# Kernel optimization log

Hardware: AMD Instinct MI355X
Metric: run time of the kernel (lower is better)

## Reference

```python
import jax, jax.numpy as jnp
import numpy as np

# static video/block geometry (matches grid_sizes = [12, 30, 50], block_layout = (3, 5, 10))
F_, H_, W_ = 12, 30, 50
FB, HB, WB = 3, 5, 10
P1, P2, P3 = F_ // FB, H_ // HB, W_ // WB      # (4, 6, 5) -> 120 tokens per block
NB = FB * HB * WB                               # 150 blocks
B = 1
N = F_ * H_ * W_                                # 18000 tokens
DIM, NH = 1536, 12
HD = DIM // NH                                  # 128
CC = HD // 2                                    # 64 rotary pairs
SPLITS = (CC - 2 * (CC // 3), CC // 3, CC // 3) # (22, 21, 21) per torch split
EPS = 1e-6
MAXP = max(F_, H_, W_)


def _block_weight():
    # BlockDistanceConv3D with transform='linear': 1 - d/dmax, column-normalized (sum over dim=0)
    f, i, j = np.meshgrid(np.arange(FB), np.arange(HB), np.arange(WB), indexing='ij')
    centers = np.stack([f.ravel() + 0.5, i.ravel() + 0.5, j.ravel() + 0.5], 1).astype(np.float64)
    d = np.linalg.norm(centers[:, None] - centers[None, :], axis=-1)
    mat = 1.0 - d / d.max()
    mat = mat / mat.sum(axis=0, keepdims=True)
    return jnp.asarray(mat, jnp.float32)        # [NB, NB]

W_BLK = _block_weight()


def setup_inputs():
    key = jax.random.key(0)
    ks = jax.random.split(key, 10)
    x = jax.random.normal(ks[0], (B, N, DIM), jnp.float32)
    seq_lens = jnp.full((B,), N, jnp.int32)
    grid_sizes = jnp.tile(jnp.array([[F_, H_, W_]], jnp.int32), (B, 1))
    # rope freqs table [MAXP, CC]: per-axis sub-tables of widths SPLITS, base 1e4
    cols = []
    for sz in SPLITS:
        inv = 1.0 / (10000.0 ** (np.arange(sz, dtype=np.float64) / sz))
        cols.append(np.arange(MAXP)[:, None] * inv[None, :])
    ang = np.concatenate(cols, axis=1)
    freqs_cos = jnp.asarray(np.cos(ang), jnp.float32)
    freqs_sin = jnp.asarray(np.sin(ang), jnp.float32)
    s = 0.02
    wq = jax.random.normal(ks[1], (DIM, DIM), jnp.float32) * s
    wk = jax.random.normal(ks[2], (DIM, DIM), jnp.float32) * s
    wv = jax.random.normal(ks[3], (DIM, DIM), jnp.float32) * s
    wo = jax.random.normal(ks[4], (DIM, DIM), jnp.float32) * s
    bq = jax.random.normal(ks[5], (DIM,), jnp.float32) * 0.01
    bk = jax.random.normal(ks[6], (DIM,), jnp.float32) * 0.01
    bv = jax.random.normal(ks[7], (DIM,), jnp.float32) * 0.01
    bo = jnp.zeros((DIM,), jnp.float32)
    nq_w = 1.0 + 0.1 * jax.random.normal(ks[8], (DIM,), jnp.float32)
    nk_w = 1.0 + 0.1 * jax.random.normal(ks[9], (DIM,), jnp.float32)
    return dict(x=x, seq_lens=seq_lens, grid_sizes=grid_sizes,
                freqs_cos=freqs_cos, freqs_sin=freqs_sin,
                wq=wq, bq=bq, wk=wk, bk=bk, wv=wv, bv=bv, wo=wo, bo=bo,
                nq_w=nq_w, nk_w=nk_w)


def _rmsnorm(t, w):
    return t * jax.lax.rsqrt(jnp.mean(t * t, -1, keepdims=True) + EPS) * w


def _pos_tab(tab):
    # expand per-axis freq table into per-token table [N, CC] (f-major, then h, then w)
    c0, c1 = SPLITS[0], SPLITS[0] + SPLITS[1]
    f = jnp.broadcast_to(tab[:F_, :c0][:, None, None, :], (F_, H_, W_, SPLITS[0]))
    h = jnp.broadcast_to(tab[:H_, c0:c1][None, :, None, :], (F_, H_, W_, SPLITS[1]))
    w = jnp.broadcast_to(tab[:W_, c1:][None, None, :, :], (F_, H_, W_, SPLITS[2]))
    return jnp.concatenate([f, h, w], -1).reshape(N, CC)


def _rope(t, cos, sin):
    # complex multiply on interleaved pairs, real arithmetic: (x0+ix1)*(c+is)
    tr = t.reshape(B, N, NH, CC, 2)
    x0, x1 = tr[..., 0], tr[..., 1]
    c = cos[None, :, None, :]
    s = sin[None, :, None, :]
    return jnp.stack([x0 * c - x1 * s, x0 * s + x1 * c], -1).reshape(B, N, NH, HD)


def _to_blocks(t):
    # 'b (fb p1 hb p2 wb p3) h d -> (b h) (fb hb wb) (p1 p2 p3) d'
    t = t.reshape(B, FB, P1, HB, P2, WB, P3, NH, HD)
    t = t.transpose(0, 7, 1, 3, 5, 2, 4, 6, 8)
    return t.reshape(B * NH, NB, P1 * P2 * P3, HD)


def reference(x, seq_lens, grid_sizes, freqs_cos, freqs_sin,
              wq, bq, wk, bk, wv, bv, wo, bo, nq_w, nk_w):
    # qkv projections (float32 throughout, as torch upcasts q/k/v to float)
    q = x @ wq.T + bq
    k = x @ wk.T + bk
    v = x @ wv.T + bv
    # RMSNorm over full dim, then relu + eps (linear-attention positivity)
    q = jax.nn.relu(_rmsnorm(q, nq_w)) + EPS
    k = jax.nn.relu(_rmsnorm(k, nk_w)) + EPS
    q = q.reshape(B, N, NH, HD)
    k = k.reshape(B, N, NH, HD)
    v = v.reshape(B, N, NH, HD)
    pc, ps = _pos_tab(freqs_cos), _pos_tab(freqs_sin)
    q_rope = _rope(q, pc, ps)
    k_rope = _rope(k, pc, ps)
    qb, kb, vb, qrb, krb = map(_to_blocks, (q, k, v, q_rope, k_rope))
    # per-block linear attention state: kv[b,n] = k_rope^T @ v
    kv = jnp.einsum('bnpd,bnpe->bnde', krb, vb)           # [B*NH, NB, HD, HD]
    kv = jnp.einsum('oi,bide->bode', W_BLK, kv)            # block-distance mixing (1x1 conv)
    # normalizer: block_mix(q @ sum_p k)
    ksum = kb.sum(axis=2)                                  # [B*NH, NB, HD]
    qk = jnp.einsum('bnpd,bnd->bnp', qb, ksum)             # [B*NH, NB, P]
    norm = jnp.einsum('oi,bip->bop', W_BLK, qk)[..., None] + EPS
    out = jnp.einsum('bnpd,bnde->bnpe', qrb, kv) / norm    # [B*NH, NB, P, HD]
    # '(b h) n p d -> b (fb p1 hb p2 wb p3) (h d)'
    out = out.reshape(B, NH, FB, HB, WB, P1, P2, P3, HD)
    out = out.transpose(0, 2, 5, 3, 6, 4, 7, 1, 8).reshape(B, N, DIM)
    return out @ wo.T + bo
```

## Files before the change

kernel.cpp:

```cpp
#include <hip/hip_runtime.h>
#include <stdint.h>


typedef unsigned short u16;
typedef unsigned int   u32;

typedef _Float16 f16x8 __attribute__((ext_vector_type(8)));
typedef float    f32x4 __attribute__((ext_vector_type(4)));

#define N_TOK 18000
#define MPAD  18176
#define DIMD  1536
#define NHH   12
#define HD    128
#define CCH   64
#define QKVN  4608
#define NBLK  150
#define PBLK  120
#define EPSF  1e-6f

#define DEVFN static __device__ __forceinline__
#define AS1 __attribute__((address_space(1)))
#define AS3 __attribute__((address_space(3)))

DEVFN u16 f2h(float f){ _Float16 h = (_Float16)f; return __builtin_bit_cast(u16, h); }
DEVFN float h2f(u16 u){ _Float16 h = __builtin_bit_cast(_Float16, u); return (float)h; }
DEVFN int2 pack4h(float a,float b,float c,float d){
  int2 r;
  r.x = (int)((u32)f2h(a) | ((u32)f2h(b)<<16));
  r.y = (int)((u32)f2h(c) | ((u32)f2h(d)<<16));
  return r;
}
DEVFN int4 packi4(float4 lo4, float4 hi4){
  int2 lo = pack4h(lo4.x, lo4.y, lo4.z, lo4.w);
  int2 hi = pack4h(hi4.x, hi4.y, hi4.z, hi4.w);
  int4 r; r.x=lo.x; r.y=lo.y; r.z=hi.x; r.w=hi.y;
  return r;
}

DEVFN void gl_lds16(const u16* g, u16* l){
  __builtin_amdgcn_global_load_lds((const AS1 void*)g, (AS3 void*)l, 16, 0, 0);
}

DEVFN f32x4 mf(f16x8 a, f16x8 b, f32x4 c){
  return __builtin_amdgcn_mfma_f32_16x16x32_f16(a, b, c, 0, 0, 0);
}

DEVFN int tok_of(int b, int p){
  int fb = b/50, hb = (b/10)%5, wb = b%10;
  int p1 = p/30; int pr = p - p1*30; int p2 = pr/5, p3 = pr - p2*5;
  return (fb*4 + p1)*1500 + (hb*6 + p2)*50 + (wb*5 + p3);
}
DEVFN void tok_pos(int b, int p, int& tok, int& f, int& h2, int& w2){
  int fb = b/50, hb = (b/10)%5, wb = b%10;
  int p1 = p/30; int pr = p - p1*30; int p2 = pr/5, p3 = pr - p2*5;
  f = fb*4 + p1; h2 = hb*6 + p2; w2 = wb*5 + p3;
  tok = (f*30 + h2)*50 + w2;
}


__global__ void conv_x_k(const float* __restrict__ x, u16* __restrict__ xh){
  const long i = ((long)blockIdx.x*256 + threadIdx.x)*8;
  if (i >= (long)MPAD*DIMD) return;
  if (i < (long)N_TOK*DIMD){
    const float4 a = *(const float4*)(x + i);
    const float4 b = *(const float4*)(x + i + 4);
    *(int4*)(xh + i) = packi4(a, b);
  } else {
    *(int4*)(xh + i) = make_int4(0,0,0,0);
  }
}

__global__ void conv_w_k(const float* __restrict__ wq, const float* __restrict__ wk,
                         const float* __restrict__ wv, const float* __restrict__ wo,
                         const float* __restrict__ bq, const float* __restrict__ bk,
                         const float* __restrict__ bv,
                         u16* __restrict__ wqkvb, u16* __restrict__ wob, float* __restrict__ bqkv){
  const long i = (long)blockIdx.x*256 + threadIdx.x;
  const long idx = i*4;
  const long SQ = (long)DIMD*DIMD;
  const long WQKV = 3*SQ;
  if (idx < WQKV){
    const float* src = (idx < SQ) ? (wq + idx) : (idx < 2*SQ ? wk + (idx - SQ) : wv + (idx - 2*SQ));
    const float4 v = *(const float4*)src;
    *(int2*)(wqkvb + idx) = pack4h(v.x, v.y, v.z, v.w);
  } else if (idx < WQKV + SQ){
    const long j = idx - WQKV;
    const float4 v = *(const float4*)(wo + j);
    *(int2*)(wob + j) = pack4h(v.x, v.y, v.z, v.w);
  }
  if (i < 3*DIMD) bqkv[i] = (i < DIMD) ? bq[i] : (i < 2*DIMD ? bk[i - DIMD] : bv[i - 2*DIMD]);
}

__global__ void wblk_k(float* __restrict__ wblk, u16* __restrict__ wh){
  __shared__ double cs[NBLK];
  const int t = threadIdx.x;
  const double dmax = sqrt(101.0);
  if (t < NBLK){
    const int fi = t/50, hi = (t/10)%5, wi = t%10;
    double s = 0.0;
    for (int o = 0; o < NBLK; o++){
      const int fo = o/50, ho = (o/10)%5, wo = o%10;
      const int df = fo-fi, dh = ho-hi, dw = wo-wi;
      s += 1.0 - sqrt((double)(df*df + dh*dh + dw*dw))/dmax;
    }
    cs[t] = s;
  }
  __syncthreads();
  for (int idx = t; idx < NBLK*NBLK; idx += 256){
    const int o = idx/NBLK, i = idx%NBLK;
    const int fo = o/50, ho = (o/10)%5, wo = o%10;
    const int fi = i/50, hi = (i/10)%5, wi = i%10;
    const int df = fo-fi, dh = ho-hi, dw = wo-wi;
    const double v = 1.0 - sqrt((double)(df*df + dh*dh + dw*dw))/dmax;
    wblk[idx] = (float)(v / cs[i]);
  }
  for (int idx = t; idx < 160*160; idx += 256){
    const int o = idx/160, i = idx%160;
    u16 hv = 0;
    if (o < NBLK && i < NBLK){
      const int fo = o/50, ho = (o/10)%5, wo = o%10;
      const int fi = i/50, hi = (i/10)%5, wi = i%10;
      const int df = fo-fi, dh = ho-hi, dw = wo-wi;
      const double v = 1.0 - sqrt((double)(df*df + dh*dh + dw*dw))/dmax;
      hv = f2h((float)(v / cs[i]));
    }
    wh[idx] = hv;
  }
}


#define STG_A(bB, kt, h) { const int ko_ = (kt)*64 + (h)*32; \
  gl_lds16(Aat + offA0 + ko_, lds + (bB)*32768 + (h)*8192 + t*8); \
  gl_lds16(Aat + offA1 + ko_, lds + (bB)*32768 + (h)*8192 + t*8 + 4096); }
#define STG_B(bB, kt, h) { const int ko_ = (kt)*64 + (h)*32; \
  gl_lds16(Bat + offB0 + ko_, lds + (bB)*32768 + 16384 + (h)*8192 + t*8); \
  gl_lds16(Bat + offB1 + ko_, lds + (bB)*32768 + 16384 + (h)*8192 + t*8 + 4096); }
#define VMC(n) asm volatile("s_waitcnt vmcnt(" #n ")" ::: "memory")
#define BARR() __builtin_amdgcn_s_barrier()
#define LGK(n) { asm volatile("s_waitcnt lgkmcnt(" #n ")" ::: "memory"); \
                 __builtin_amdgcn_sched_barrier(0); }

#define RD_A4(dst, bB, kk, mlo) { \
  _Pragma("unroll") for (int i_=0;i_<4;i_++) \
    dst[i_] = *(const f16x8*)(lds + (bB)*32768 + (kk)*8192 + arow + ((mlo)+i_)*512); }
#define RD_B4(dst, bB, kk) { \
  _Pragma("unroll") for (int i_=0;i_<4;i_++) \
    dst[i_] = *(const f16x8*)(lds + (bB)*32768 + 16384 + (kk)*8192 + brow + i_*512); }
#define MM4(mlo, aR, bR) { \
  __builtin_amdgcn_s_setprio(1); \
  _Pragma("unroll") for (int i_=0;i_<4;i_++){ \
    acc[(mlo)+i_][0] = mf(aR[i_], bR[0], acc[(mlo)+i_][0]); \
    acc[(mlo)+i_][1] = mf(aR[i_], bR[1], acc[(mlo)+i_][1]); \
    acc[(mlo)+i_][2] = mf(aR[i_], bR[2], acc[(mlo)+i_][2]); \
    acc[(mlo)+i_][3] = mf(aR[i_], bR[3], acc[(mlo)+i_][3]); } \
  __builtin_amdgcn_s_setprio(0); }

#define TILE4(bB, S1, S2, S3, S4, VM) { \
  RD_A4(aA, bB, 0, 0); RD_B4(bX, bB, 0); RD_A4(aB, bB, 0, 4); \
  S1; LGK(4); MM4(0, aA, bX); BARR(); \
  RD_A4(aA, bB, 1, 0); RD_B4(bY, bB, 1); \
  S2; LGK(8); MM4(4, aB, bX); BARR(); \
  RD_A4(aB, bB, 1, 4); \
  S3; LGK(4); MM4(0, aA, bY); BARR(); \
  S4; VM; LGK(0); MM4(4, aB, bY); BARR(); }

DEVFN void gemm256_core(const u16* __restrict__ Aat, const u16* __restrict__ Bat,
                        u16* lds, long row0, long col0, int K, f32x4 (&acc)[8][4]){
  const int t = threadIdx.x;
  const int lane = t&63, lr = lane&15;
  const int q = lane>>4;
  const int w = t>>6, wr = w>>2, wc = w&3;
  const int slot8 = (q ^ ((lr>>1)&3))*8;
  const int arow = (wr*128 + lr)*32 + slot8;
  const int brow = (wc*64 + lr)*32 + slot8;
  const int s1 = t + 512;
  const int r0 = t>>2, r1 = s1>>2;
  const int g0 = ((t&3)  ^ ((r0>>1)&3))*8;
  const int g1 = ((s1&3) ^ ((r1>>1)&3))*8;
  const long offA0 = (row0 + r0)*(long)K + g0, offA1 = (row0 + r1)*(long)K + g1;
  const long offB0 = (col0 + r0)*(long)K + g0, offB1 = (col0 + r1)*(long)K + g1;

  f16x8 aA[4], aB[4], bX[4], bY[4];
  STG_A(0,0,0); STG_B(0,0,0); STG_A(0,0,1); STG_B(0,0,1);
  STG_A(1,1,0); STG_B(1,1,0);
  VMC(4); BARR();

  const int NIT = K/128;
#pragma unroll 1
  for (int j = 0; j < NIT-1; ++j){
    const int c1 = 2*j+1, p0 = 2*j+2, p1 = 2*j+3;
    TILE4(0, STG_A(1,c1,1), STG_B(1,c1,1), STG_A(0,p0,0), STG_B(0,p0,0), VMC(4));
    TILE4(1, STG_A(0,p0,1), STG_B(0,p0,1), STG_A(1,p1,0), STG_B(1,p1,0), VMC(4));
  }
  { const int cL1 = 2*(K/128)-1;
    TILE4(0, STG_A(1,cL1,1), STG_B(1,cL1,1), (void)0, (void)0, VMC(0));
    TILE4(1, (void)0, (void)0, (void)0, (void)0, (void)0);
  }
}

__global__ __launch_bounds__(512, 2) void gemm_qkv256(const u16* __restrict__ A, const u16* __restrict__ B,
                                                      const float* __restrict__ bias,
                                                      u16* __restrict__ qb, u16* __restrict__ kb,
                                                      u16* __restrict__ vb){
  __shared__ u16 lds[65536];
  const int bn = blockIdx.x, bm = blockIdx.y;
  const long row0 = (long)bm*256, col0 = (long)bn*256;
  f32x4 acc[8][4] = {};
  gemm256_core(A, B, lds, row0, col0, DIMD, acc);

  const int t = threadIdx.x, lane = t&63, lr = lane&15, q = lane>>4;
  const int w = t>>6, wr = w>>2, wc = w&3;
  const int which = bn/6;
  u16* dst = (which == 0) ? qb : (which == 1 ? kb : vb);
  const int lcol0 = (bn - which*6)*256 + wc*64;
  const int gcol0 = bn*256 + wc*64;
#pragma unroll
  for (int nt = 0; nt < 4; nt++){
    const float bb = bias[gcol0 + nt*16 + lr];
    const int col = lcol0 + nt*16 + lr;
#pragma unroll
    for (int mt = 0; mt < 8; mt++)
#pragma unroll
      for (int r = 0; r < 4; r++){
        const long rr = row0 + wr*128 + mt*16 + q*4 + r;
        if (rr < N_TOK) dst[rr*DIMD + col] = f2h(acc[mt][nt][r] + bb);
      }
  }
}

__global__ __launch_bounds__(512, 2) void gemm_bt256(const u16* __restrict__ A, const u16* __restrict__ B,
                                                     const float* __restrict__ bias, float* __restrict__ C){
  __shared__ u16 lds[65536];
  const int bn = blockIdx.x, bm = blockIdx.y;
  const long row0 = (long)bm*256, col0 = (long)bn*256;
  f32x4 acc[8][4] = {};
  gemm256_core(A, B, lds, row0, col0, DIMD, acc);

  const int t = threadIdx.x, lane = t&63, lr = lane&15, q = lane>>4;
  const int w = t>>6, wr = w>>2, wc = w&3;
#pragma unroll
  for (int nt = 0; nt < 4; nt++){
    const int col = bn*256 + wc*64 + nt*16 + lr;
    const float bb = bias[col];
#pragma unroll
    for (int mt = 0; mt < 8; mt++)
#pragma unroll
      for (int r = 0; r < 4; r++){
        const long rr = row0 + wr*128 + mt*16 + q*4 + r;
        if (rr < N_TOK) C[rr*DIMD + col] = acc[mt][nt][r] + bb;
      }
  }
}

__global__ __launch_bounds__(256) void norm_k(u16* __restrict__ qb, u16* __restrict__ kb,
                                              const float* __restrict__ nqw, const float* __restrict__ nkw){
  __shared__ float red[4];
  __shared__ float s_scale;
  const int n = blockIdx.x, t = threadIdx.x, lane = t&63, wv = t>>6;
  u16* bufs[2]; bufs[0] = qb; bufs[1] = kb;
  const float* wgts[2]; wgts[0] = nqw; wgts[1] = nkw;
  for (int pass = 0; pass < 2; pass++){
    u16* row = bufs[pass] + (long)n*DIMD;
    const float* wgt = wgts[pass];
    float v[6];
    float ssq = 0.f;
#pragma unroll
    for (int i = 0; i < 6; i++){ v[i] = h2f(row[t + i*256]); ssq += v[i]*v[i]; }
#pragma unroll
    for (int o = 32; o > 0; o >>= 1) ssq += __shfl_down(ssq, o);
    if (lane == 0) red[wv] = ssq;
    __syncthreads();
    if (t == 0) s_scale = rsqrtf((red[0]+red[1]+red[2]+red[3])/(float)DIMD + EPSF);
    __syncthreads();
    const float sc = s_scale;
#pragma unroll
    for (int i = 0; i < 6; i++){
      float r = fmaxf(v[i]*sc*wgt[t + i*256], 0.f) + EPSF;
      row[t + i*256] = f2h(r);
    }
    __syncthreads();
  }
}

__global__ __launch_bounds__(128) void ksum_k(const u16* __restrict__ kb, float* __restrict__ ksum){
  const int hb = blockIdx.x; const int h = hb/NBLK, b = hb%NBLK; const int d = threadIdx.x;
  float s = 0.f;
  for (int p = 0; p < PBLK; p++)
    s += h2f(kb[(long)tok_of(b, p)*DIMD + h*HD + d]);
  ksum[(long)hb*HD + d] = s;
}

__global__ __launch_bounds__(128) void qk_k(const u16* __restrict__ qb, const float* __restrict__ ksum,
                                            float* __restrict__ qk){
  __shared__ float ks[HD];
  const int hb = blockIdx.x, h = hb/NBLK, b = hb%NBLK, t = threadIdx.x;
  ks[t] = ksum[(long)hb*HD + t];
  __syncthreads();
  if (t < PBLK){
    const u16* row = qb + (long)tok_of(b, t)*DIMD + h*HD;
    float s = 0.f;
#pragma unroll
    for (int d8 = 0; d8 < 16; d8++){
      int4 v4 = *(const int4*)(row + d8*8);
      const u16* pv = (const u16*)&v4;
#pragma unroll
      for (int j = 0; j < 8; j++) s += h2f(pv[j])*ks[d8*8 + j];
    }
    qk[(long)hb*PBLK + t] = s;
  }
}

__global__ __launch_bounds__(128) void mixqk_k(const float* __restrict__ qk, const float* __restrict__ wblk,
                                               float* __restrict__ nrm){
  const int ho = blockIdx.x, h = ho/NBLK, o = ho%NBLK, t = threadIdx.x;
  if (t >= PBLK) return;
  float s = 0.f;
  for (int i = 0; i < NBLK; i++) s += wblk[o*NBLK + i]*qk[((long)h*NBLK + i)*PBLK + t];
  nrm[(long)ho*PBLK + t] = s + EPSF;
}

__global__ __launch_bounds__(256) void kv_k(const u16* __restrict__ kb, const u16* __restrict__ vb,
                                            const float* __restrict__ fcos, const float* __restrict__ fsin,
                                            u16* __restrict__ kv1){
  __shared__ u16 Ap[4][128][32];
  __shared__ u16 Bp[4][128][32];
  const int hb = blockIdx.x, h = hb/NBLK, b = hb%NBLK, t = threadIdx.x;
  for (int idx = t; idx < 128*64; idx += 256){
    const int p = idx>>6, cc = idx&63;
    u16 v0=0, v1=0, r0=0, r1=0;
    if (p < PBLK){
      int tok, f, hh, ww; tok_pos(b, p, tok, f, hh, ww);
      const long tb = (long)tok*DIMD + h*HD + 2*cc;
      const u32 vv = *(const u32*)&vb[tb];
      const u32 kk = *(const u32*)&kb[tb];
      const int pos = (cc < 22) ? f : (cc < 43 ? hh : ww);
      const float cv = fcos[pos*CCH + cc], sv = fsin[pos*CCH + cc];
      const float x0 = h2f((u16)kk), x1 = h2f((u16)(kk>>16));
      v0 = (u16)vv; v1 = (u16)(vv>>16);
      r0 = f2h(x0*cv - x1*sv); r1 = f2h(x0*sv + x1*cv);
    }
    const int kp = p>>5, j = p&31;
    Ap[kp][2*cc][j] = v0; Ap[kp][2*cc+1][j] = v1;
    Bp[kp][2*cc][j] = r0; Bp[kp][2*cc+1][j] = r1;
  }
  __syncthreads();
  const int wave = t>>6, lane = t&63, lr = lane&15, quad = lane>>4;
  const int wm = (wave&1)*64, wn = (wave>>1)*64;
  f32x4 acc[4][4] = {};
#pragma unroll
  for (int kp = 0; kp < 4; kp++){
    f16x8 aF[4], bF[4];
#pragma unroll
    for (int mt = 0; mt < 4; mt++) aF[mt] = *(const f16x8*)&Ap[kp][wm + mt*16 + lr][quad*8];
#pragma unroll
    for (int nt = 0; nt < 4; nt++) bF[nt] = *(const f16x8*)&Bp[kp][wn + nt*16 + lr][quad*8];
#pragma unroll
    for (int mt = 0; mt < 4; mt++)
#pragma unroll
      for (int nt = 0; nt < 4; nt++)
        acc[mt][nt] = __builtin_amdgcn_mfma_f32_16x16x32_f16(aF[mt], bF[nt], acc[mt][nt], 0, 0, 0);
  }
  u16* outp = kv1 + (long)hb*HD*HD;
#pragma unroll
  for (int mt = 0; mt < 4; mt++)
#pragma unroll
    for (int nt = 0; nt < 4; nt++)
#pragma unroll
      for (int r = 0; r < 4; r++)
        outp[(wm + mt*16 + quad*4 + r)*HD + wn + nt*16 + lr] = f2h(acc[mt][nt][r]);
}

__global__ __launch_bounds__(256) void mix_gemm(const u16* __restrict__ kv1, const u16* __restrict__ wh,
                                                u16* __restrict__ kv2){
  __shared__ u16 Xs[5][128][32];
  const int h = blockIdx.y, jc = blockIdx.x, t = threadIdx.x;
  const long base = (long)h*NBLK*HD*HD + jc*128;
#pragma unroll
  for (int it = 0; it < 10; it++){
    const int idx = t + it*256;
    const int i = idx>>4, jg = idx&15;
    int4 v = make_int4(0,0,0,0);
    if (i < NBLK) v = *(const int4*)&kv1[base + (long)i*HD*HD + jg*8];
    const u16* pv = (const u16*)&v;
    const int kp = i>>5, il = i&31;
    const int ib = ((((il>>3) ^ jg) & 3)<<3) | (il&7);
#pragma unroll
    for (int e = 0; e < 8; e++) Xs[kp][jg*8 + e][ib] = pv[e];
  }
  __syncthreads();
  const int wave = t>>6, lane = t&63, lr = lane&15, quad = lane>>4;
  const int wm = (wave&1)*80, wn = (wave>>1)*64;
  f32x4 acc[5][4] = {};
#pragma unroll
  for (int kp = 0; kp < 5; kp++){
    f16x8 aF[5], bF[4];
#pragma unroll
    for (int mt = 0; mt < 5; mt++)
      aF[mt] = *(const f16x8*)&wh[(wm + mt*16 + lr)*160 + kp*32 + quad*8];
#pragma unroll
    for (int nt = 0; nt < 4; nt++){
      const int j = wn + nt*16 + lr;
      bF[nt] = *(const f16x8*)&Xs[kp][j][((quad ^ (j>>3)) & 3)<<3];
    }
#pragma unroll
    for (int mt = 0; mt < 5; mt++)
#pragma unroll
      for (int nt = 0; nt < 4; nt++)
        acc[mt][nt] = __builtin_amdgcn_mfma_f32_16x16x32_f16(aF[mt], bF[nt], acc[mt][nt], 0, 0, 0);
  }
#pragma unroll
  for (int mt = 0; mt < 5; mt++)
#pragma unroll
    for (int nt = 0; nt < 4; nt++)
#pragma unroll
      for (int r = 0; r < 4; r++){
        const int o = wm + mt*16 + quad*4 + r;
        if (o < NBLK)
          kv2[(long)(h*NBLK + o)*HD*HD + jc*128 + wn + nt*16 + lr] = f2h(acc[mt][nt][r]);
      }
}

__global__ __launch_bounds__(256) void attn_k(const u16* __restrict__ qb, const u16* __restrict__ kv2,
                                              const float* __restrict__ fcos, const float* __restrict__ fsin,
                                              const float* __restrict__ nrm, u16* __restrict__ aout){
  __shared__ u16 Ap[4][128][32];
  __shared__ u16 Bp[4][128][32];
  const int ho = blockIdx.x, h = ho/NBLK, o = ho%NBLK, t = threadIdx.x;
  for (int idx = t; idx < 128*64; idx += 256){
    const int p = idx>>6, cc = idx&63;
    u32 w = 0;
    if (p < PBLK){
      int tok, f, hh, ww; tok_pos(o, p, tok, f, hh, ww);
      const u32 qq = *(const u32*)&qb[(long)tok*DIMD + h*HD + 2*cc];
      const int pos = (cc < 22) ? f : (cc < 43 ? hh : ww);
      const float cv = fcos[pos*CCH + cc], sv = fsin[pos*CCH + cc];
      const float x0 = h2f((u16)qq), x1 = h2f((u16)(qq>>16));
      w = (u32)f2h(x0*cv - x1*sv) | ((u32)f2h(x0*sv + x1*cv) << 16);
    }
    *(u32*)&Ap[(2*cc)>>5][p][(2*cc)&31] = w;
  }
  const u16* kv2p = kv2 + (long)ho*HD*HD;
  for (int idx = t; idx < 128*16; idx += 256){
    const int e = idx>>4, d8 = (idx&15)*8;
    int4 vv = *(const int4*)&kv2p[e*HD + d8];
    *(int4*)&Bp[d8>>5][e][d8&31] = vv;
  }
  __syncthreads();
  const int wave = t>>6, lane = t&63, lr = lane&15, quad = lane>>4;
  const int wm = (wave&1)*64, wn = (wave>>1)*64;
  f32x4 acc[4][4] = {};
#pragma unroll
  for (int kp = 0; kp < 4; kp++){
    f16x8 aF[4], bF[4];
#pragma unroll
    for (int mt = 0; mt < 4; mt++) aF[mt] = *(const f16x8*)&Ap[kp][wm + mt*16 + lr][quad*8];
#pragma unroll
    for (int nt = 0; nt < 4; nt++) bF[nt] = *(const f16x8*)&Bp[kp][wn + nt*16 + lr][quad*8];
#pragma unroll
    for (int mt = 0; mt < 4; mt++)
#pragma unroll
      for (int nt = 0; nt < 4; nt++)
        acc[mt][nt] = __builtin_amdgcn_mfma_f32_16x16x32_f16(aF[mt], bF[nt], acc[mt][nt], 0, 0, 0);
  }
#pragma unroll
  for (int mt = 0; mt < 4; mt++)
#pragma unroll
    for (int r = 0; r < 4; r++){
      const int p = wm + mt*16 + quad*4 + r;
      if (p >= PBLK) continue;
      const float inv = 1.0f / nrm[(long)ho*PBLK + p];
      const long tb = (long)tok_of(o, p)*DIMD + h*HD;
#pragma unroll
      for (int nt = 0; nt < 4; nt++)
        aout[tb + wn + nt*16 + lr] = f2h(acc[mt][nt][r]*inv);
    }
}

extern "C" void kernel_launch(void* const* d_in, const int* in_sizes, int n_in,
                              void* d_out, int out_size, void* d_ws, size_t ws_size,
                              hipStream_t stream){
  const float* x    = (const float*)d_in[0];
  const float* fcos = (const float*)d_in[3];
  const float* fsin = (const float*)d_in[4];
  const float* wq   = (const float*)d_in[5];
  const float* bq   = (const float*)d_in[6];
  const float* wk   = (const float*)d_in[7];
  const float* bk   = (const float*)d_in[8];
  const float* wv   = (const float*)d_in[9];
  const float* bv   = (const float*)d_in[10];
  const float* wo   = (const float*)d_in[11];
  const float* bo   = (const float*)d_in[12];
  const float* nqw  = (const float*)d_in[13];
  const float* nkw  = (const float*)d_in[14];
  float* out = (float*)d_out;
  (void)in_sizes; (void)n_in; (void)out_size; (void)ws_size;

  char* ws = (char*)d_ws; size_t off = 0;
  auto alloc = [&](size_t b)->void*{ void* p = ws + off; off += (b + 255) & ~(size_t)255; return p; };
  const size_t SQ = (size_t)DIMD*DIMD;
  u16*   wqkvb = (u16*)  alloc(3*SQ*2);
  u16*   wob   = (u16*)  alloc(SQ*2);
  float* bqkv  = (float*)alloc((size_t)3*DIMD*4);
  float* wblk  = (float*)alloc((size_t)NBLK*NBLK*4);
  u16*   wh    = (u16*)  alloc((size_t)160*160*2);
  u16*   qb    = (u16*)  alloc((size_t)MPAD*DIMD*2);
  u16*   kb    = (u16*)  alloc((size_t)MPAD*DIMD*2);
  u16*   vb    = (u16*)  alloc((size_t)MPAD*DIMD*2);
  u16*   kv1   = (u16*)  alloc((size_t)NHH*NBLK*HD*HD*2);
  float* ksum  = (float*)alloc((size_t)NHH*NBLK*HD*4);
  float* qk    = (float*)alloc((size_t)NHH*NBLK*PBLK*4);
  float* nrm   = (float*)alloc((size_t)NHH*NBLK*PBLK*4);
  u16*   kv2   = kb;
  u16*   xh    = kv1;

  conv_w_k<<<9216, 256, 0, stream>>>(wq, wk, wv, wo, bq, bk, bv, wqkvb, wob, bqkv);
  wblk_k<<<1, 256, 0, stream>>>(wblk, wh);
  conv_x_k<<<(MPAD*DIMD/8 + 255)/256, 256, 0, stream>>>(x, xh);
  gemm_qkv256<<<dim3(QKVN/256, MPAD/256), 512, 0, stream>>>(xh, wqkvb, bqkv, qb, kb, vb);
  norm_k<<<N_TOK, 256, 0, stream>>>(qb, kb, nqw, nkw);
  ksum_k<<<NHH*NBLK, 128, 0, stream>>>(kb, ksum);
  qk_k<<<NHH*NBLK, 128, 0, stream>>>(qb, ksum, qk);
  mixqk_k<<<NHH*NBLK, 128, 0, stream>>>(qk, wblk, nrm);
  kv_k<<<NHH*NBLK, 256, 0, stream>>>(kb, vb, fcos, fsin, kv1);
  mix_gemm<<<dim3(HD*HD/128, NHH), 256, 0, stream>>>(kv1, wh, kv2);
  attn_k<<<NHH*NBLK, 256, 0, stream>>>(qb, kv2, fcos, fsin, nrm, qb);
  gemm_bt256<<<dim3(DIMD/256, MPAD/256), 512, 0, stream>>>(qb, wob, bo, out);
}
```

Before: 1.048 ms.

## Reschedule GEMM LDS reads, vectorize norm, parallelize ksum and wblk kernels

Reorders the GEMM inner tile so the LDS fragment reads for the next step are issued right after each MFMA group, with barriers and a full lgkmcnt wait before each group. This is meant to overlap LDS latency with MFMA work. Separately, the RMS norm kernel now uses 192 threads with 128-bit vectorized loads and stores. The k-sum kernel now splits the token reduction across 8 groups with a shared-memory final reduce, and the block-weight kernel runs across 40 blocks instead of one. Each block still recomputes the column sums. The extra barriers in the GEMM could add synchronization stalls.

```diff
diff --git a/kernel.cpp b/kernel.cpp
--- a/kernel.cpp
+++ b/kernel.cpp
@@ -107,7 +107,7 @@
     cs[t] = s;
   }
   __syncthreads();
-  for (int idx = t; idx < NBLK*NBLK; idx += 256){
+  for (int idx = blockIdx.x*256 + t; idx < NBLK*NBLK; idx += gridDim.x*256){
     const int o = idx/NBLK, i = idx%NBLK;
     const int fo = o/50, ho = (o/10)%5, wo = o%10;
     const int fi = i/50, hi = (i/10)%5, wi = i%10;
@@ -115,7 +115,7 @@
     const double v = 1.0 - sqrt((double)(df*df + dh*dh + dw*dw))/dmax;
     wblk[idx] = (float)(v / cs[i]);
   }
-  for (int idx = t; idx < 160*160; idx += 256){
+  for (int idx = blockIdx.x*256 + t; idx < 160*160; idx += gridDim.x*256){
     const int o = idx/160, i = idx%160;
     u16 hv = 0;
     if (o < NBLK && i < NBLK){
@@ -138,7 +138,7 @@
   gl_lds16(Bat + offB1 + ko_, lds + (bB)*32768 + 16384 + (h)*8192 + t*8 + 4096); }
 #define VMC(n) asm volatile("s_waitcnt vmcnt(" #n ")" ::: "memory")
 #define BARR() __builtin_amdgcn_s_barrier()
-#define LGK(n) { asm volatile("s_waitcnt lgkmcnt(" #n ")" ::: "memory"); \
+#define LGK0() { asm volatile("s_waitcnt lgkmcnt(0)" ::: "memory"); \
                  __builtin_amdgcn_sched_barrier(0); }
 
 #define RD_A4(dst, bB, kk, mlo) { \
@@ -156,14 +156,13 @@
     acc[(mlo)+i_][3] = mf(aR[i_], bR[3], acc[(mlo)+i_][3]); } \
   __builtin_amdgcn_s_setprio(0); }
 
-#define TILE4(bB, S1, S2, S3, S4, VM) { \
-  RD_A4(aA, bB, 0, 0); RD_B4(bX, bB, 0); RD_A4(aB, bB, 0, 4); \
-  S1; LGK(4); MM4(0, aA, bX); BARR(); \
-  RD_A4(aA, bB, 1, 0); RD_B4(bY, bB, 1); \
-  S2; LGK(8); MM4(4, aB, bX); BARR(); \
-  RD_A4(aB, bB, 1, 4); \
-  S3; LGK(4); MM4(0, aA, bY); BARR(); \
-  S4; VM; LGK(0); MM4(4, aB, bY); BARR(); }
+#define TILE4(bB, S1, S2, S3, S4, VM, RDN) { \
+  S1; BARR(); LGK0(); MM4(0, aA, bX); RD_A4(aB, bB, 0, 4); BARR(); \
+  S2; BARR(); LGK0(); MM4(4, aB, bX); RD_A4(aA, bB, 1, 0); RD_B4(bY, bB, 1); BARR(); \
+  S3; BARR(); LGK0(); MM4(0, aA, bY); RD_A4(aB, bB, 1, 4); BARR(); \
+  S4; VM; BARR(); LGK0(); MM4(4, aB, bY); RDN; BARR(); }
+
+#define RDN0(bB) { RD_A4(aA, bB, 0, 0); RD_B4(bX, bB, 0); }
 
 DEVFN void gemm256_core(const u16* __restrict__ Aat, const u16* __restrict__ Bat,
                         u16* lds, long row0, long col0, int K, f32x4 (&acc)[8][4]){
@@ -185,17 +184,18 @@
   STG_A(0,0,0); STG_B(0,0,0); STG_A(0,0,1); STG_B(0,0,1);
   STG_A(1,1,0); STG_B(1,1,0);
   VMC(4); BARR();
+  RDN0(0);
 
   const int NIT = K/128;
 #pragma unroll 1
   for (int j = 0; j < NIT-1; ++j){
     const int c1 = 2*j+1, p0 = 2*j+2, p1 = 2*j+3;
-    TILE4(0, STG_A(1,c1,1), STG_B(1,c1,1), STG_A(0,p0,0), STG_B(0,p0,0), VMC(4));
-    TILE4(1, STG_A(0,p0,1), STG_B(0,p0,1), STG_A(1,p1,0), STG_B(1,p1,0), VMC(4));
+    TILE4(0, STG_A(1,c1,1), STG_B(1,c1,1), STG_A(0,p0,0), STG_B(0,p0,0), VMC(4), RDN0(1));
+    TILE4(1, STG_A(0,p0,1), STG_B(0,p0,1), STG_A(1,p1,0), STG_B(1,p1,0), VMC(4), RDN0(0));
   }
   { const int cL1 = 2*(K/128)-1;
-    TILE4(0, STG_A(1,cL1,1), STG_B(1,cL1,1), (void)0, (void)0, VMC(0));
-    TILE4(1, (void)0, (void)0, (void)0, (void)0, (void)0);
+    TILE4(0, STG_A(1,cL1,1), STG_B(1,cL1,1), (void)0, (void)0, VMC(0), RDN0(1));
+    TILE4(1, (void)0, (void)0, (void)0, (void)0, (void)0, (void)0);
   }
 }
 
@@ -253,9 +253,9 @@
   }
 }
 
-__global__ __launch_bounds__(256) void norm_k(u16* __restrict__ qb, u16* __restrict__ kb,
+__global__ __launch_bounds__(192) void norm_k(u16* __restrict__ qb, u16* __restrict__ kb,
                                               const float* __restrict__ nqw, const float* __restrict__ nkw){
-  __shared__ float red[4];
+  __shared__ float red[3];
   __shared__ float s_scale;
   const int n = blockIdx.x, t = threadIdx.x, lane = t&63, wv = t>>6;
   u16* bufs[2]; bufs[0] = qb; bufs[1] = kb;
@@ -263,32 +263,51 @@
   for (int pass = 0; pass < 2; pass++){
     u16* row = bufs[pass] + (long)n*DIMD;
     const float* wgt = wgts[pass];
-    float v[6];
+    int4 v4 = *(const int4*)(row + t*8);
+    const u16* pv = (const u16*)&v4;
+    float v[8];
     float ssq = 0.f;
 #pragma unroll
-    for (int i = 0; i < 6; i++){ v[i] = h2f(row[t + i*256]); ssq += v[i]*v[i]; }
+    for (int i = 0; i < 8; i++){ v[i] = h2f(pv[i]); ssq += v[i]*v[i]; }
 #pragma unroll
     for (int o = 32; o > 0; o >>= 1) ssq += __shfl_down(ssq, o);
     if (lane == 0) red[wv] = ssq;
     __syncthreads();
-    if (t == 0) s_scale = rsqrtf((red[0]+red[1]+red[2]+red[3])/(float)DIMD + EPSF);
+    if (t == 0) s_scale = rsqrtf((red[0]+red[1]+red[2])/(float)DIMD + EPSF);
     __syncthreads();
     const float sc = s_scale;
-#pragma unroll
-    for (int i = 0; i < 6; i++){
-      float r = fmaxf(v[i]*sc*wgt[t + i*256], 0.f) + EPSF;
-      row[t + i*256] = f2h(r);
-    }
+    const float4 w0 = *(const float4*)(wgt + t*8);
+    const float4 w1 = *(const float4*)(wgt + t*8 + 4);
+    const float wa[8] = {w0.x,w0.y,w0.z,w0.w,w1.x,w1.y,w1.z,w1.w};
+    u16 o8[8];
+#pragma unroll
+    for (int i = 0; i < 8; i++)
+      o8[i] = f2h(fmaxf(v[i]*sc*wa[i], 0.f) + EPSF);
+    *(int4*)(row + t*8) = *(const int4*)o8;
     __syncthreads();
   }
 }
 
-__global__ __launch_bounds__(128) void ksum_k(const u16* __restrict__ kb, float* __restrict__ ksum){
-  const int hb = blockIdx.x; const int h = hb/NBLK, b = hb%NBLK; const int d = threadIdx.x;
-  float s = 0.f;
-  for (int p = 0; p < PBLK; p++)
-    s += h2f(kb[(long)tok_of(b, p)*DIMD + h*HD + d]);
-  ksum[(long)hb*HD + d] = s;
+__global__ __launch_bounds__(256) void ksum_k(const u16* __restrict__ kb, float* __restrict__ ksum){
+  __shared__ float red[8][HD];
+  const int hb = blockIdx.x; const int h = hb/NBLK, b = hb%NBLK, t = threadIdx.x;
+  const int pg = t>>5, dl = t&31;
+  float s0=0.f, s1=0.f, s2=0.f, s3=0.f;
+  for (int i = 0; i < 15; i++){
+    const int p = pg*15 + i;
+    const u16* r = kb + (long)tok_of(b, p)*DIMD + h*HD + dl*4;
+    int2 v = *(const int2*)r;
+    const u16* pv = (const u16*)&v;
+    s0 += h2f(pv[0]); s1 += h2f(pv[1]); s2 += h2f(pv[2]); s3 += h2f(pv[3]);
+  }
+  red[pg][dl*4+0]=s0; red[pg][dl*4+1]=s1; red[pg][dl*4+2]=s2; red[pg][dl*4+3]=s3;
+  __syncthreads();
+  if (t < HD){
+    float s = 0.f;
+#pragma unroll
+    for (int g = 0; g < 8; g++) s += red[g][t];
+    ksum[(long)hb*HD + t] = s;
+  }
 }
 
 __global__ __launch_bounds__(128) void qk_k(const u16* __restrict__ qb, const float* __restrict__ ksum,
@@ -515,11 +534,11 @@
   u16*   xh    = kv1;
 
   conv_w_k<<<9216, 256, 0, stream>>>(wq, wk, wv, wo, bq, bk, bv, wqkvb, wob, bqkv);
-  wblk_k<<<1, 256, 0, stream>>>(wblk, wh);
+  wblk_k<<<40, 256, 0, stream>>>(wblk, wh);
   conv_x_k<<<(MPAD*DIMD/8 + 255)/256, 256, 0, stream>>>(x, xh);
   gemm_qkv256<<<dim3(QKVN/256, MPAD/256), 512, 0, stream>>>(xh, wqkvb, bqkv, qb, kb, vb);
-  norm_k<<<N_TOK, 256, 0, stream>>>(qb, kb, nqw, nkw);
-  ksum_k<<<NHH*NBLK, 128, 0, stream>>>(kb, ksum);
+  norm_k<<<N_TOK, 192, 0, stream>>>(qb, kb, nqw, nkw);
+  ksum_k<<<NHH*NBLK, 256, 0, stream>>>(kb, ksum);
   qk_k<<<NHH*NBLK, 128, 0, stream>>>(qb, ksum, qk);
   mixqk_k<<<NHH*NBLK, 128, 0, stream>>>(qk, wblk, nrm);
   kv_k<<<NHH*NBLK, 256, 0, stream>>>(kb, vb, fcos, fsin, kv1);
```

Result: faster. 996.5 us (-4.9%).
